# Kernel tuning notes

Hardware: AMD Instinct MI355X
Metric: run time of the kernel (lower is better)

## Reference

```python
import jax, jax.numpy as jnp
import numpy as np

B, T, C = 4, 2048, 2048
H, D, L = 16, 128, 512


def _rope(x, cos, sin):
    # x: [B, T, H, D]; cos/sin: [T, D//2]; consecutive-pair complex rotation
    x2 = x.reshape(*x.shape[:-1], -1, 2)
    x0, x1 = x2[..., 0], x2[..., 1]
    c = cos[None, :, None, :]
    s = sin[None, :, None, :]
    o0 = x0 * c - x1 * s
    o1 = x0 * s + x1 * c
    return jnp.stack([o0, o1], axis=-1).reshape(x.shape)


def setup_inputs() -> dict:
    key = jax.random.key(0)
    ks = jax.random.split(key, 8)
    x = jax.random.normal(ks[0], (B, T, C), dtype=jnp.float32)
    # rotary table, theta = 10000
    inv_freq = 1.0 / (10000.0 ** (np.arange(0, D, 2, dtype=np.float32) / D))
    ang = np.outer(np.arange(T, dtype=np.float32), inv_freq)
    freqs_cos = jnp.asarray(np.cos(ang), dtype=jnp.float32)
    freqs_sin = jnp.asarray(np.sin(ang), dtype=jnp.float32)
    sc = 0.02
    wq = sc * jax.random.normal(ks[1], (H * D, C), dtype=jnp.float32)
    wkv_down = sc * jax.random.normal(ks[2], (L, C), dtype=jnp.float32)
    wk_up = sc * jax.random.normal(ks[3], (D, L), dtype=jnp.float32)
    wv_up = sc * jax.random.normal(ks[4], (D, L), dtype=jnp.float32)
    wo = sc * jax.random.normal(ks[5], (C, H * D), dtype=jnp.float32)
    return {"x": x, "freqs_cos": freqs_cos, "freqs_sin": freqs_sin,
            "wq": wq, "wkv_down": wkv_down, "wk_up": wk_up,
            "wv_up": wv_up, "wo": wo}


def reference(x, freqs_cos, freqs_sin, wq, wkv_down, wk_up, wv_up, wo):
    Bc, Tc, Cc = x.shape
    # query projection -> [B, T, H, D]
    q = jnp.einsum('btc,ec->bte', x, wq).reshape(Bc, Tc, H, D)
    # shared latent KV: [B, T, L]
    kv_latent = jnp.einsum('btc,lc->btl', x, wkv_down)
    # up-project to single shared head: [B, T, D]
    k = jnp.einsum('btl,dl->btd', kv_latent, wk_up)
    v = jnp.einsum('btl,dl->btd', kv_latent, wv_up)
    # RoPE on q (per head) and k (single shared head)
    q = _rope(q, freqs_cos, freqs_sin)
    k = _rope(k[:, :, None, :], freqs_cos, freqs_sin)[:, :, 0, :]
    # causal SDPA; k/v are shared across heads (MLA) so avoid expanding them
    scale = 1.0 / jnp.sqrt(jnp.asarray(D, dtype=x.dtype))
    scores = jnp.einsum('bthd,bsd->bhts', q, k) * scale  # [B, H, T, S]
    causal = jnp.tril(jnp.ones((Tc, Tc), dtype=bool))
    scores = jnp.where(causal[None, None, :, :], scores, jnp.finfo(x.dtype).min)
    probs = jax.nn.softmax(scores, axis=-1)
    y = jnp.einsum('bhts,bsd->bthd', probs, v).reshape(Bc, Tc, H * D)
    return jnp.einsum('bte,ce->btc', y, wo)
```

## Files before the change

kernel.cpp:

```cpp
#include <hip/hip_runtime.h>
#include <hip/hip_bf16.h>
#include <cstddef>

#define BB 4
#define TT 2048
#define CC 2048
#define HH 16
#define DD 128
#define LL 512

typedef _Float16 f16;
typedef f16 f16x2 __attribute__((ext_vector_type(2)));
typedef f16 f16x4 __attribute__((ext_vector_type(4)));
typedef f16 f16x8 __attribute__((ext_vector_type(8)));
typedef float f32x4 __attribute__((ext_vector_type(4)));

__device__ __forceinline__ void async_load16(void* lptr, const void* gptr) {
  __builtin_amdgcn_global_load_lds(
      (const __attribute__((address_space(1))) unsigned int*)gptr,
      (__attribute__((address_space(3))) unsigned int*)lptr, 16, 0, 0);
}

template <int EPI>
__global__ __launch_bounds__(512, 2) void mla_gemm_256(
    const f16* __restrict__ A, const f16* __restrict__ B,
    void* __restrict__ Cv, int M, int N, int K,
    const float* __restrict__ cosb, const float* __restrict__ sinb) {
  __shared__ __align__(16) f16 smem[2][2][256 * 64];

  const int tid = threadIdx.x;
  const int lane = tid & 63;
  const int w = tid >> 6;
  const int lnm = lane & 15, quad = lane >> 4;
  const int wm = w >> 2, wn = w & 3;

  const int nwg = gridDim.x;
  const int bid0 = blockIdx.x;
  const int q8 = nwg >> 3, r8 = nwg & 7;
  const int xcd = bid0 & 7, lid = bid0 >> 3;
  const int wg =
      (xcd < r8 ? xcd * (q8 + 1) : r8 * (q8 + 1) + (xcd - r8) * q8) + lid;
  const int ntc = N >> 8;
  const int m0 = (wg / ntc) * 256;
  const int n0 = (wg % ntc) * 256;

  const int srow = tid >> 3;
  const int sch = (tid & 7) ^ ((tid >> 3) & 7);
  const f16* Ag = A + (size_t)(m0 + srow) * K + sch * 8;
  const f16* Bg = B + (size_t)(n0 + srow) * K + sch * 8;

  auto stage = [&](int bi, int k0, int h) {
    const int mat = h >> 1;
    const int rb = (h & 1) * 128;
    const f16* g = (mat ? Bg : Ag) + (size_t)rb * K + k0;
    f16* l = &smem[bi][mat][rb * 64 + tid * 8];
    async_load16(l, g);
    async_load16(l + 4096, g + (size_t)64 * K);
  };

  const int rx8 = lnm & 7;
  auto rdA = [&](const f16* Ab, int i, int ks) -> f16x8 {
    return *(const f16x8*)&Ab[(wm * 128 + i * 16 + lnm) * 64 +
                              (((ks * 4 + quad) ^ rx8) * 8)];
  };
  auto rdB = [&](const f16* Bb, int j, int ks) -> f16x8 {
    return *(const f16x8*)&Bb[(wn * 64 + j * 16 + lnm) * 64 +
                              (((ks * 4 + quad) ^ rx8) * 8)];
  };

  f32x4 acc[8][4] = {};

  const int NT = K >> 6;

  stage(0, 0, 0);
  stage(0, 0, 1);
  stage(0, 0, 2);
  stage(0, 0, 3);
  stage(1, 64, 0);
  asm volatile("s_waitcnt vmcnt(2)" ::: "memory");
  __builtin_amdgcn_s_barrier();

  for (int t = 0; t < NT; ++t) {
    const int bi = t & 1;
    const f16* Ab = smem[bi][0];
    const f16* Bb = smem[bi][1];
    const int k1 = (t + 1 < NT ? t + 1 : t) << 6;
    const int k2 = (t + 2 < NT ? t + 2 : t) << 6;

    f16x8 Ar[4][2], Br[2][2];

#pragma unroll
    for (int i = 0; i < 4; i++)
#pragma unroll
      for (int ks = 0; ks < 2; ks++) Ar[i][ks] = rdA(Ab, i, ks);
#pragma unroll
    for (int j = 0; j < 2; j++)
#pragma unroll
      for (int ks = 0; ks < 2; ks++) Br[j][ks] = rdB(Bb, j, ks);
    stage(bi ^ 1, k1, 1);
    __builtin_amdgcn_s_barrier();
    asm volatile("s_waitcnt lgkmcnt(0)" ::: "memory");
    __builtin_amdgcn_s_setprio(1);
#pragma unroll
    for (int i = 0; i < 4; i++)
#pragma unroll
      for (int j = 0; j < 2; j++)
#pragma unroll
        for (int ks = 0; ks < 2; ks++)
          acc[i][j] = __builtin_amdgcn_mfma_f32_16x16x32_f16(
              Ar[i][ks], Br[j][ks], acc[i][j], 0, 0, 0);
    __builtin_amdgcn_s_setprio(0);
    __builtin_amdgcn_s_barrier();

#pragma unroll
    for (int j = 0; j < 2; j++)
#pragma unroll
      for (int ks = 0; ks < 2; ks++) Br[j][ks] = rdB(Bb, 2 + j, ks);
    stage(bi ^ 1, k1, 2);
    __builtin_amdgcn_s_barrier();
    asm volatile("s_waitcnt lgkmcnt(0)" ::: "memory");
    __builtin_amdgcn_s_setprio(1);
#pragma unroll
    for (int i = 0; i < 4; i++)
#pragma unroll
      for (int j = 0; j < 2; j++)
#pragma unroll
        for (int ks = 0; ks < 2; ks++)
          acc[i][2 + j] = __builtin_amdgcn_mfma_f32_16x16x32_f16(
              Ar[i][ks], Br[j][ks], acc[i][2 + j], 0, 0, 0);
    __builtin_amdgcn_s_setprio(0);
    __builtin_amdgcn_s_barrier();

#pragma unroll
    for (int i = 0; i < 4; i++)
#pragma unroll
      for (int ks = 0; ks < 2; ks++) Ar[i][ks] = rdA(Ab, 4 + i, ks);
    stage(bi ^ 1, k1, 3);
    __builtin_amdgcn_s_barrier();
    asm volatile("s_waitcnt lgkmcnt(0)" ::: "memory");
    __builtin_amdgcn_s_setprio(1);
#pragma unroll
    for (int i = 0; i < 4; i++)
#pragma unroll
      for (int j = 0; j < 2; j++)
#pragma unroll
        for (int ks = 0; ks < 2; ks++)
          acc[4 + i][2 + j] = __builtin_amdgcn_mfma_f32_16x16x32_f16(
              Ar[i][ks], Br[j][ks], acc[4 + i][2 + j], 0, 0, 0);
    __builtin_amdgcn_s_setprio(0);
    __builtin_amdgcn_s_barrier();

#pragma unroll
    for (int j = 0; j < 2; j++)
#pragma unroll
      for (int ks = 0; ks < 2; ks++) Br[j][ks] = rdB(Bb, j, ks);
    stage(bi, k2, 0);
    __builtin_amdgcn_s_barrier();
    asm volatile("s_waitcnt lgkmcnt(0)" ::: "memory");
    __builtin_amdgcn_s_setprio(1);
#pragma unroll
    for (int i = 0; i < 4; i++)
#pragma unroll
      for (int j = 0; j < 2; j++)
#pragma unroll
        for (int ks = 0; ks < 2; ks++)
          acc[4 + i][j] = __builtin_amdgcn_mfma_f32_16x16x32_f16(
              Ar[i][ks], Br[j][ks], acc[4 + i][j], 0, 0, 0);
    __builtin_amdgcn_s_setprio(0);
    asm volatile("s_waitcnt vmcnt(2)" ::: "memory");
    __builtin_amdgcn_s_barrier();
  }

  asm volatile("s_waitcnt vmcnt(0)" ::: "memory");

  if constexpr (EPI == 0) {
    float* C = (float*)Cv;
#pragma unroll
    for (int i = 0; i < 8; i++)
#pragma unroll
      for (int r = 0; r < 4; r++) {
        float* crow = C + (size_t)(m0 + wm * 128 + i * 16 + quad * 4 + r) * N +
                      n0 + wn * 64 + lnm;
#pragma unroll
        for (int j = 0; j < 4; j++) crow[j * 16] = acc[i][j][r];
      }
  } else {
    f16* C = (f16*)Cv;
    const float SCLQ = 0.1275174280f;
#pragma unroll
    for (int i = 0; i < 8; i++)
#pragma unroll
      for (int r = 0; r < 4; r++) {
        const int m = m0 + wm * 128 + i * 16 + quad * 4 + r;
        const int t = m & (TT - 1);
#pragma unroll
        for (int j = 0; j < 4; j++) {
          const int col = n0 + wn * 64 + j * 16 + lnm;
          float v = acc[i][j][r];
          float u = __shfl_xor(v, 1, 64);
          const int fi = (col & (DD - 1)) >> 1;
          const float ct = cosb[t * (DD / 2) + fi];
          const float st2 = sinb[t * (DD / 2) + fi];
          const float o =
              (lnm & 1) ? (u * st2 + v * ct) : (v * ct - u * st2);
          C[(size_t)m * N + col] = (f16)(o * SCLQ);
        }
      }
  }
}

__global__ __launch_bounds__(256) void mla_gemm_mfma_h(
    const f16* __restrict__ A, const f16* __restrict__ B,
    f16* __restrict__ C, int M, int N, int K) {
  __shared__ f16 As[128 * 32];
  __shared__ f16 Bs[128 * 32];

  const int tid = threadIdx.x;
  const int lane = tid & 63;
  const int w = tid >> 6;
  const int lnm = lane & 15, quad = lane >> 4;
  const int wm = w >> 1, wn = w & 1;
  const int m0 = blockIdx.y * 128;
  const int n0 = blockIdx.x * 128;

  const int srow = tid >> 2;
  const int skoff = (tid & 3) * 8;

  f32x4 acc[4][4] = {};

  for (int k0 = 0; k0 < K; k0 += 32) {
    const f16* ag = A + (size_t)(m0 + srow) * K + k0 + skoff;
    const f16* bg = B + (size_t)(n0 + srow) * K + k0 + skoff;
    async_load16(&As[(size_t)tid * 8], ag);
    async_load16(&As[(size_t)(256 + tid) * 8], ag + (size_t)64 * K);
    async_load16(&Bs[(size_t)tid * 8], bg);
    async_load16(&Bs[(size_t)(256 + tid) * 8], bg + (size_t)64 * K);
    __syncthreads();

    f16x8 af[4], bf[4];
#pragma unroll
    for (int i = 0; i < 4; i++)
      af[i] = *(const f16x8*)&As[(wm * 64 + i * 16 + lnm) * 32 + quad * 8];
#pragma unroll
    for (int j = 0; j < 4; j++)
      bf[j] = *(const f16x8*)&Bs[(wn * 64 + j * 16 + lnm) * 32 + quad * 8];
#pragma unroll
    for (int i = 0; i < 4; i++)
#pragma unroll
      for (int j = 0; j < 4; j++)
        acc[i][j] = __builtin_amdgcn_mfma_f32_16x16x32_f16(af[i], bf[j],
                                                           acc[i][j], 0, 0, 0);
    __syncthreads();
  }

#pragma unroll
  for (int i = 0; i < 4; i++)
#pragma unroll
    for (int r = 0; r < 4; r++) {
      f16* crow = C + (size_t)(m0 + wm * 64 + i * 16 + quad * 4 + r) * N +
                  n0 + wn * 64 + lnm;
#pragma unroll
      for (int j = 0; j < 4; j++) crow[j * 16] = (f16)acc[i][j][r];
    }
}

__global__ __launch_bounds__(256) void mla_gemm_upkv(
    const f16* __restrict__ A, const f16* __restrict__ B,
    f16* __restrict__ khp, f16* __restrict__ vtp,
    const float* __restrict__ cosb, const float* __restrict__ sinb) {
  const int NN = 256, KK = 512;
  (void)NN;
  __shared__ f16 As[128 * 32];
  __shared__ f16 Bs[128 * 32];

  const int tid = threadIdx.x;
  const int lane = tid & 63;
  const int w = tid >> 6;
  const int lnm = lane & 15, quad = lane >> 4;
  const int wm = w >> 1, wn = w & 1;
  const int m0 = blockIdx.y * 128;
  const int n0 = blockIdx.x * 128;

  const int srow = tid >> 2;
  const int skoff = (tid & 3) * 8;

  f32x4 acc[4][4] = {};

  for (int k0 = 0; k0 < KK; k0 += 32) {
    const f16* ag = A + (size_t)(m0 + srow) * KK + k0 + skoff;
    const f16* bg = B + (size_t)(n0 + srow) * KK + k0 + skoff;
    async_load16(&As[(size_t)tid * 8], ag);
    async_load16(&As[(size_t)(256 + tid) * 8], ag + (size_t)64 * KK);
    async_load16(&Bs[(size_t)tid * 8], bg);
    async_load16(&Bs[(size_t)(256 + tid) * 8], bg + (size_t)64 * KK);
    __syncthreads();

    f16x8 af[4], bf[4];
#pragma unroll
    for (int i = 0; i < 4; i++)
      af[i] = *(const f16x8*)&As[(wm * 64 + i * 16 + lnm) * 32 + quad * 8];
#pragma unroll
    for (int j = 0; j < 4; j++)
      bf[j] = *(const f16x8*)&Bs[(wn * 64 + j * 16 + lnm) * 32 + quad * 8];
#pragma unroll
    for (int i = 0; i < 4; i++)
#pragma unroll
      for (int j = 0; j < 4; j++)
        acc[i][j] = __builtin_amdgcn_mfma_f32_16x16x32_f16(af[i], bf[j],
                                                           acc[i][j], 0, 0, 0);
    __syncthreads();
  }

  const bool isv = (n0 != 0);
#pragma unroll
  for (int i = 0; i < 4; i++)
#pragma unroll
    for (int r = 0; r < 4; r++) {
      const int m = m0 + wm * 64 + i * 16 + quad * 4 + r;
      const int b = m >> 11, t = m & (TT - 1);
      const int st = t >> 6, s = t & 63;
      if (!isv) {
        f16* tb = khp + (size_t)(b * 32 + st) * 8192;
#pragma unroll
        for (int j = 0; j < 4; j++) {
          const int n = wn * 64 + j * 16 + lnm;
          float v = acc[i][j][r];
          float u = __shfl_xor(v, 1, 64);
          const int fi = n >> 1;
          const float ct = cosb[t * 64 + fi];
          const float st2 = sinb[t * 64 + fi];
          const float o = (lnm & 1) ? (u * st2 + v * ct) : (v * ct - u * st2);
          tb[(n >> 3) * 512 + s * 8 + (n & 7)] = (f16)o;
        }
      } else {
        const int cq2 = ((s >> 5) << 2) | ((s >> 2) & 3);
        const int e = (((s >> 4) & 1) << 2) | (s & 3);
        f16* tb = vtp + (size_t)(b * 32 + st) * 8192 + cq2 * 1024 + e;
#pragma unroll
        for (int j = 0; j < 4; j++) {
          const int d = wn * 64 + j * 16 + lnm;
          tb[d * 8] = (f16)acc[i][j][r];
        }
      }
    }
}

#define CVT_C0 ((size_t)BB * TT * CC)
#define CVT_C1 (CVT_C0 + (size_t)CC * CC)
#define CVT_C2 (CVT_C1 + (size_t)LL * CC)
#define CVT_C3 (CVT_C2 + (size_t)DD * LL)
#define CVT_C4 (CVT_C3 + (size_t)DD * LL)
#define CVT_C5 (CVT_C4 + (size_t)CC * CC)
__global__ __launch_bounds__(256) void mla_cvt_all(
    const float* __restrict__ x, const float* __restrict__ wq,
    const float* __restrict__ wdn, const float* __restrict__ wku,
    const float* __restrict__ wvu, const float* __restrict__ wo,
    f16* __restrict__ dst) {
  size_t i4 = (size_t)blockIdx.x * 256 + threadIdx.x;
  if (i4 >= CVT_C5 / 4) return;
  size_t e = i4 * 4;
  const float* src;
  size_t off;
  if (e < CVT_C0) { src = x; off = e; }
  else if (e < CVT_C1) { src = wq; off = e - CVT_C0; }
  else if (e < CVT_C2) { src = wdn; off = e - CVT_C1; }
  else if (e < CVT_C3) { src = wku; off = e - CVT_C2; }
  else if (e < CVT_C4) { src = wvu; off = e - CVT_C3; }
  else { src = wo; off = e - CVT_C4; }
  float4 v = *(const float4*)&src[off];
  f16x4 r = {(f16)v.x, (f16)v.y, (f16)v.z, (f16)v.w};
  *(f16x4*)(dst + e) = r;
}

__global__ __launch_bounds__(256, 3) void mla_flash2(
    const f16* __restrict__ qh, const f16* __restrict__ khp,
    const f16* __restrict__ vtp, f16* __restrict__ y) {
  __shared__ __align__(16) f16 Ks[2][8192];
  __shared__ __align__(16) f16 Vs[8192];

  const int tid = threadIdx.x;
  const int lane = tid & 63;
  const int w = tid >> 6;
  const int lnm = lane & 15, quad = lane >> 4;

  const int bid = blockIdx.x;
  const int qt = (TT / 128 - 1) - (bid >> 6);
  const int bh = bid & 63;
  const int b = bh >> 4, h = bh & 15;
  const int q0b = qt * 128;
  const int q0 = q0b + w * 32;

  f16x8 qf[2][4];
#pragma unroll
  for (int qnb = 0; qnb < 2; qnb++) {
    const f16* qrow =
        qh + ((size_t)(b * TT + q0 + qnb * 16 + lnm) * HH + h) * DD;
#pragma unroll
    for (int c = 0; c < 4; c++)
      qf[qnb][c] = *(const f16x8*)(qrow + c * 32 + quad * 8);
  }

  f32x4 O[2][8] = {};
  float l_acc[2] = {0.f, 0.f};

  const int nst = (q0b + 128) / 64;
  const int wmax = q0 + 31;
  const f16* kpb = khp + (size_t)b * 32 * 8192;
  const f16* vpb = vtp + (size_t)b * 32 * 8192;

  auto stageK = [&](int buf, int st) {
    const f16* g = kpb + (size_t)st * 8192 + (size_t)tid * 8;
#pragma unroll
    for (int i = 0; i < 4; i++)
      async_load16(&Ks[buf][(size_t)(i * 256 + tid) * 8], g + i * 2048);
  };
  auto stageV = [&](int st) {
    const f16* g = vpb + (size_t)st * 8192 + (size_t)tid * 8;
#pragma unroll
    for (int i = 0; i < 4; i++)
      async_load16(&Vs[(size_t)(i * 256 + tid) * 8], g + i * 2048);
  };

  const int kbo = quad * 512 + lnm * 8;
  const int vbo = quad * 1024 + lnm * 8;

  stageK(0, 0);
  stageV(0);
  __syncthreads();

  for (int st = 0; st < nst; st++) {
    const int cur = st & 1;
    const int s0 = st * 64;
    if (st + 1 < nst) stageK(cur ^ 1, st + 1);

    const bool act = (s0 <= wmax);
    f16x8 P8[2][2];
    if (act) {
      const f16* kl = &Ks[cur][kbo];
      f32x4 S[2][4] = {};
      __builtin_amdgcn_s_setprio(1);
#pragma unroll
      for (int sb = 0; sb < 4; sb++)
#pragma unroll
        for (int c = 0; c < 4; c++) {
          f16x8 ka = *(const f16x8*)&kl[c * 2048 + sb * 128];
          S[0][sb] = __builtin_amdgcn_mfma_f32_16x16x32_f16(ka, qf[0][c],
                                                            S[0][sb], 0, 0, 0);
          S[1][sb] = __builtin_amdgcn_mfma_f32_16x16x32_f16(ka, qf[1][c],
                                                            S[1][sb], 0, 0, 0);
        }
      __builtin_amdgcn_s_setprio(0);

      const bool domask = (s0 + 63 > q0);
      if (!domask) {
#pragma unroll
        for (int qnb = 0; qnb < 2; qnb++) {
          float lp = 0.f;
#pragma unroll
          for (int sb = 0; sb < 4; sb++)
#pragma unroll
            for (int j = 0; j < 4; j++) {
              float p = __builtin_amdgcn_exp2f(S[qnb][sb][j]);
              lp += p;
              P8[qnb][sb >> 1][(sb & 1) * 4 + j] = (f16)p;
            }
          l_acc[qnb] += lp;
        }
      } else {
#pragma unroll
        for (int qnb = 0; qnb < 2; qnb++) {
          const int m_abs = q0 + qnb * 16 + lnm;
          float lp = 0.f;
#pragma unroll
          for (int sb = 0; sb < 4; sb++) {
            const int srow = s0 + sb * 16 + quad * 4;
#pragma unroll
            for (int j = 0; j < 4; j++) {
              float p = __builtin_amdgcn_exp2f(S[qnb][sb][j]);
              if (srow + j > m_abs) p = 0.f;
              lp += p;
              P8[qnb][sb >> 1][(sb & 1) * 4 + j] = (f16)p;
            }
          }
          l_acc[qnb] += lp;
        }
      }
    }

    __syncthreads();

    if (act) {
      const f16* vl = &Vs[vbo];
      __builtin_amdgcn_s_setprio(1);
#pragma unroll
      for (int c = 0; c < 2; c++)
#pragma unroll
        for (int db = 0; db < 8; db++) {
          f16x8 vb = *(const f16x8*)&vl[c * 4096 + db * 128];
          O[0][db] = __builtin_amdgcn_mfma_f32_16x16x32_f16(P8[0][c], vb,
                                                            O[0][db], 0, 0, 0);
          O[1][db] = __builtin_amdgcn_mfma_f32_16x16x32_f16(P8[1][c], vb,
                                                            O[1][db], 0, 0, 0);
        }
      __builtin_amdgcn_s_setprio(0);
    }

    __syncthreads();
    if (st + 1 < nst) stageV(st + 1);
  }

#pragma unroll
  for (int qnb = 0; qnb < 2; qnb++) {
    float l = l_acc[qnb];
    l += __shfl_xor(l, 16, 64);
    l += __shfl_xor(l, 32, 64);
    l_acc[qnb] = l;
  }

#pragma unroll
  for (int qnb = 0; qnb < 2; qnb++) {
    float linv[4];
#pragma unroll
    for (int r = 0; r < 4; r++)
      linv[r] = 1.f / __shfl(l_acc[qnb], quad * 4 + r, 64);
#pragma unroll
    for (int db = 0; db < 8; db++)
#pragma unroll
      for (int r = 0; r < 4; r++) {
        size_t off =
            ((size_t)(b * TT + q0 + qnb * 16 + quad * 4 + r) * HH + h) * DD +
            db * 16 + lnm;
        y[off] = (f16)(O[qnb][db][r] * linv[r]);
      }
  }
}

extern "C" void kernel_launch(void* const* d_in, const int* in_sizes, int n_in,
                              void* d_out, int out_size, void* d_ws,
                              size_t ws_size, hipStream_t stream) {
  const float* x      = (const float*)d_in[0];
  const float* fcos   = (const float*)d_in[1];
  const float* fsin   = (const float*)d_in[2];
  const float* wq     = (const float*)d_in[3];
  const float* wkv_dn = (const float*)d_in[4];
  const float* wk_up  = (const float*)d_in[5];
  const float* wv_up  = (const float*)d_in[6];
  const float* wo     = (const float*)d_in[7];
  float* out = (float*)d_out;

  const int M = BB * TT;

  float* ws = (float*)d_ws;
  float* qbuf   = ws;
  f16*   xh     = (f16*)(qbuf + (size_t)M * CC);
  f16*   wqh    = xh + (size_t)M * CC;
  f16*   wdownh = wqh + (size_t)CC * CC;
  f16*   wkvuph = wdownh + (size_t)LL * CC;
  f16*   woh    = wkvuph + (size_t)256 * LL;
  f16*   kvh    = woh + (size_t)CC * CC;
  f16*   khp    = kvh + (size_t)M * LL;
  f16*   vtp    = khp + (size_t)M * DD;
  f16*   qh     = (f16*)qbuf;
  f16*   yh     = qh + (size_t)M * CC;

  {
    size_t total4 = CVT_C5 / 4;
    mla_cvt_all<<<(unsigned)((total4 + 255) / 256), dim3(256), 0, stream>>>(
        x, wq, wkv_dn, wk_up, wv_up, wo, xh);
  }

  mla_gemm_256<1><<<dim3((M / 256) * (CC / 256)), dim3(512), 0, stream>>>(
      xh, wqh, qh, M, CC, CC, fcos, fsin);

  mla_gemm_mfma_h<<<dim3(LL / 128, M / 128), dim3(256), 0, stream>>>(
      xh, wdownh, kvh, M, LL, CC);

  mla_gemm_upkv<<<dim3(2, M / 128), dim3(256), 0, stream>>>(
      kvh, wkvuph, khp, vtp, fcos, fsin);

  mla_flash2<<<dim3(BB * HH * (TT / 128)), dim3(256), 0, stream>>>(
      qh, khp, vtp, yh);

  mla_gemm_256<0><<<dim3((M / 256) * (CC / 256)), dim3(512), 0, stream>>>(
      yh, woh, out, M, CC, CC, nullptr, nullptr);
}
```

Before: 417.3 us.

## Remap warp sub-tiles to quadrant layout and restage loads per quadrant

Changes the 256x256 GEMM so that each warp's 8x4 sub-tiles are spread across four 128x128 quadrants rather than forming one contiguous 128x64 block. The per-phase staging order now matches which quadrant is consumed next. All four half-tiles of the next K step are issued within the current iteration, replacing the old scheme that prefetched two steps ahead, and vmcnt waits now sit between phases. The aim is to shorten the wait before the first MFMA phase and spread LDS readiness across the iteration, at the cost of a shallower prefetch depth and more waitcnt points.

```diff
diff --git a/kernel.cpp b/kernel.cpp
--- a/kernel.cpp
+++ b/kernel.cpp
@@ -59,12 +59,12 @@
   };
 
   const int rx8 = lnm & 7;
-  auto rdA = [&](const f16* Ab, int i, int ks) -> f16x8 {
-    return *(const f16x8*)&Ab[(wm * 128 + i * 16 + lnm) * 64 +
+  auto rdA = [&](const f16* Ab, int mq, int i, int ks) -> f16x8 {
+    return *(const f16x8*)&Ab[(mq * 128 + wm * 64 + i * 16 + lnm) * 64 +
                               (((ks * 4 + quad) ^ rx8) * 8)];
   };
-  auto rdB = [&](const f16* Bb, int j, int ks) -> f16x8 {
-    return *(const f16x8*)&Bb[(wn * 64 + j * 16 + lnm) * 64 +
+  auto rdB = [&](const f16* Bb, int nq, int j, int ks) -> f16x8 {
+    return *(const f16x8*)&Bb[(nq * 128 + wn * 32 + j * 16 + lnm) * 64 +
                               (((ks * 4 + quad) ^ rx8) * 8)];
   };
 
@@ -73,11 +73,10 @@
   const int NT = K >> 6;
 
   stage(0, 0, 0);
-  stage(0, 0, 1);
   stage(0, 0, 2);
   stage(0, 0, 3);
-  stage(1, 64, 0);
-  asm volatile("s_waitcnt vmcnt(2)" ::: "memory");
+  stage(0, 0, 1);
+  asm volatile("s_waitcnt vmcnt(4)" ::: "memory");
   __builtin_amdgcn_s_barrier();
 
   for (int t = 0; t < NT; ++t) {
@@ -85,19 +84,18 @@
     const f16* Ab = smem[bi][0];
     const f16* Bb = smem[bi][1];
     const int k1 = (t + 1 < NT ? t + 1 : t) << 6;
-    const int k2 = (t + 2 < NT ? t + 2 : t) << 6;
 
     f16x8 Ar[4][2], Br[2][2];
 
 #pragma unroll
     for (int i = 0; i < 4; i++)
 #pragma unroll
-      for (int ks = 0; ks < 2; ks++) Ar[i][ks] = rdA(Ab, i, ks);
+      for (int ks = 0; ks < 2; ks++) Ar[i][ks] = rdA(Ab, 0, i, ks);
 #pragma unroll
     for (int j = 0; j < 2; j++)
 #pragma unroll
-      for (int ks = 0; ks < 2; ks++) Br[j][ks] = rdB(Bb, j, ks);
-    stage(bi ^ 1, k1, 1);
+      for (int ks = 0; ks < 2; ks++) Br[j][ks] = rdB(Bb, 0, j, ks);
+    stage(bi ^ 1, k1, 0);
     __builtin_amdgcn_s_barrier();
     asm volatile("s_waitcnt lgkmcnt(0)" ::: "memory");
     __builtin_amdgcn_s_setprio(1);
@@ -110,12 +108,13 @@
           acc[i][j] = __builtin_amdgcn_mfma_f32_16x16x32_f16(
               Ar[i][ks], Br[j][ks], acc[i][j], 0, 0, 0);
     __builtin_amdgcn_s_setprio(0);
+    asm volatile("s_waitcnt vmcnt(4)" ::: "memory");
     __builtin_amdgcn_s_barrier();
 
 #pragma unroll
     for (int j = 0; j < 2; j++)
 #pragma unroll
-      for (int ks = 0; ks < 2; ks++) Br[j][ks] = rdB(Bb, 2 + j, ks);
+      for (int ks = 0; ks < 2; ks++) Br[j][ks] = rdB(Bb, 1, j, ks);
     stage(bi ^ 1, k1, 2);
     __builtin_amdgcn_s_barrier();
     asm volatile("s_waitcnt lgkmcnt(0)" ::: "memory");
@@ -129,12 +128,13 @@
           acc[i][2 + j] = __builtin_amdgcn_mfma_f32_16x16x32_f16(
               Ar[i][ks], Br[j][ks], acc[i][2 + j], 0, 0, 0);
     __builtin_amdgcn_s_setprio(0);
-    __builtin_amdgcn_s_barrier();
-
-#pragma unroll
-    for (int i = 0; i < 4; i++)
-#pragma unroll
-      for (int ks = 0; ks < 2; ks++) Ar[i][ks] = rdA(Ab, 4 + i, ks);
+    asm volatile("s_waitcnt vmcnt(4)" ::: "memory");
+    __builtin_amdgcn_s_barrier();
+
+#pragma unroll
+    for (int i = 0; i < 4; i++)
+#pragma unroll
+      for (int ks = 0; ks < 2; ks++) Ar[i][ks] = rdA(Ab, 1, i, ks);
     stage(bi ^ 1, k1, 3);
     __builtin_amdgcn_s_barrier();
     asm volatile("s_waitcnt lgkmcnt(0)" ::: "memory");
@@ -153,8 +153,8 @@
 #pragma unroll
     for (int j = 0; j < 2; j++)
 #pragma unroll
-      for (int ks = 0; ks < 2; ks++) Br[j][ks] = rdB(Bb, j, ks);
-    stage(bi, k2, 0);
+      for (int ks = 0; ks < 2; ks++) Br[j][ks] = rdB(Bb, 0, j, ks);
+    stage(bi ^ 1, k1, 1);
     __builtin_amdgcn_s_barrier();
     asm volatile("s_waitcnt lgkmcnt(0)" ::: "memory");
     __builtin_amdgcn_s_setprio(1);
@@ -167,7 +167,7 @@
           acc[4 + i][j] = __builtin_amdgcn_mfma_f32_16x16x32_f16(
               Ar[i][ks], Br[j][ks], acc[4 + i][j], 0, 0, 0);
     __builtin_amdgcn_s_setprio(0);
-    asm volatile("s_waitcnt vmcnt(2)" ::: "memory");
+    asm volatile("s_waitcnt vmcnt(4)" ::: "memory");
     __builtin_amdgcn_s_barrier();
   }
 
@@ -176,27 +176,34 @@
   if constexpr (EPI == 0) {
     float* C = (float*)Cv;
 #pragma unroll
-    for (int i = 0; i < 8; i++)
+    for (int I = 0; I < 8; I++) {
+      const int mq = I >> 2, ii = I & 3;
 #pragma unroll
       for (int r = 0; r < 4; r++) {
-        float* crow = C + (size_t)(m0 + wm * 128 + i * 16 + quad * 4 + r) * N +
-                      n0 + wn * 64 + lnm;
-#pragma unroll
-        for (int j = 0; j < 4; j++) crow[j * 16] = acc[i][j][r];
+        const int row = m0 + mq * 128 + wm * 64 + ii * 16 + quad * 4 + r;
+#pragma unroll
+        for (int J = 0; J < 4; J++) {
+          const int nq = J >> 1, jj = J & 1;
+          const int col = n0 + nq * 128 + wn * 32 + jj * 16 + lnm;
+          C[(size_t)row * N + col] = acc[I][J][r];
+        }
       }
+    }
   } else {
     f16* C = (f16*)Cv;
     const float SCLQ = 0.1275174280f;
 #pragma unroll
-    for (int i = 0; i < 8; i++)
+    for (int I = 0; I < 8; I++) {
+      const int mq = I >> 2, ii = I & 3;
 #pragma unroll
       for (int r = 0; r < 4; r++) {
-        const int m = m0 + wm * 128 + i * 16 + quad * 4 + r;
+        const int m = m0 + mq * 128 + wm * 64 + ii * 16 + quad * 4 + r;
         const int t = m & (TT - 1);
 #pragma unroll
-        for (int j = 0; j < 4; j++) {
-          const int col = n0 + wn * 64 + j * 16 + lnm;
-          float v = acc[i][j][r];
+        for (int J = 0; J < 4; J++) {
+          const int nq = J >> 1, jj = J & 1;
+          const int col = n0 + nq * 128 + wn * 32 + jj * 16 + lnm;
+          float v = acc[I][J][r];
           float u = __shfl_xor(v, 1, 64);
           const int fi = (col & (DD - 1)) >> 1;
           const float ct = cosb[t * (DD / 2) + fi];
@@ -206,6 +213,7 @@
           C[(size_t)m * N + col] = (f16)(o * SCLQ);
         }
       }
+    }
   }
 }
 
@@ -268,8 +276,7 @@
     const f16* __restrict__ A, const f16* __restrict__ B,
     f16* __restrict__ khp, f16* __restrict__ vtp,
     const float* __restrict__ cosb, const float* __restrict__ sinb) {
-  const int NN = 256, KK = 512;
-  (void)NN;
+  const int KK = 512;
   __shared__ f16 As[128 * 32];
   __shared__ f16 Bs[128 * 32];
 
```

Measured after the change: 428.5 us. 2.7% more time.
